# Kernel tuning notes

Measured on AMD Instinct MI355X. Metric: run time of the kernel, lower is better.

Reference implementation:

```python
import jax, jax.numpy as jnp
import numpy as np

N = 32768
F0, F1, F2, F3 = 16, 32, 64, 128
D0, D1, D2, D3 = (128, 128, 128), (64, 64, 64), (32, 32, 32), (16, 16, 16)
DST1, DST2, DTF = (16, 16, 16, 64), (64, 64, 32, 16), (4, 4, 4, 65536)
FST1, FST2, FTF = 64, 8, 8
TOTAL = 7 * (F0 + F1 + F2 + F3) + 9 * FST1 + 9 * FST2 + FTF  # 2336
INNER = 64
FACE3 = np.array([[1,0,0],[-1,0,0],[0,1,0],[0,-1,0],[0,0,1],[0,0,-1]], np.int32)
ST8 = np.concatenate([np.concatenate([FACE3, np.zeros((6,1), np.int32)], 1),
                      np.array([[0,0,0,1],[0,0,0,-1]], np.int32)], 0)

def rmsnorm(x, scale, eps=1e-8):
    rms = jnp.sqrt(jnp.mean(x * x, axis=-1, keepdims=True))
    return scale * x / (rms + eps)

def geglu(x):
    a, g = jnp.split(x, 2, axis=-1)
    return a * jax.nn.gelu(g)

def table_feats(table, p, offsets):
    # p in [0,1)^D -> scaled integer indices; gather base + modulo-wrapped neighbors
    dims = np.array(table.shape[:-1], np.int32)
    idx = (p * (dims - 1)).astype(jnp.int32)  # [N, D]
    base = table[tuple(idx[:, i] for i in range(idx.shape[-1]))]  # [N, F]
    if offsets is None:
        return base
    nbr = (idx[:, None, :] + offsets[None]) % dims  # [N, K, D]
    nf = table[tuple(nbr[..., i] for i in range(nbr.shape[-1]))]  # [N, K, F]
    return jnp.concatenate([base, nf.reshape(nf.shape[0], -1)], axis=-1)

def setup_inputs():
    key = jax.random.key(0)
    ks = jax.random.split(key, 20)
    tbl = lambda k, dims, f: jax.random.normal(k, dims + (f,), jnp.float32) * 0.1
    lin = lambda k, i, o: jax.random.normal(k, (i, o), jnp.float32) / np.sqrt(i).astype(np.float32)
    return dict(
        pos=jax.random.normal(ks[0], (N, 3), jnp.float32),
        dir=jax.random.normal(ks[1], (N, 3), jnp.float32),
        t=jax.random.uniform(ks[2], (N,), jnp.float32),
        table0=tbl(ks[3], D0, F0), table1=tbl(ks[4], D1, F1),
        table2=tbl(ks[5], D2, F2), table3=tbl(ks[6], D3, F3),
        st1=tbl(ks[7], DST1, FST1), st2=tbl(ks[8], DST2, FST2), tf=tbl(ks[9], DTF, FTF),
        sph_proj=lin(ks[10], 3, 8), tb1=jnp.zeros((1,), jnp.float32), tb2=jnp.zeros((1,), jnp.float32),
        gn1=jnp.ones((12,), jnp.float32), gw1=lin(ks[11], 12, 32),
        gn2=jnp.ones((16,), jnp.float32), gw2=lin(ks[12], 16, 32),
        gn3=jnp.ones((16,), jnp.float32), gw3=lin(ks[13], 16, 3),
        vn1=jnp.ones((TOTAL,), jnp.float32), vw1=lin(ks[14], TOTAL, 2 * TOTAL),
        vn2=jnp.ones((TOTAL,), jnp.float32), vw2=lin(ks[15], TOTAL, INNER),
        fw=lin(ks[16], INNER + 4, 4), fb=jnp.zeros((4,), jnp.float32))

def _forward(pos, dir, t, table0, table1, table2, table3, st1, st2, tf,
             sph_proj, tb1, tb2, gn1, gw1, gn2, gw2, gn3, gw3,
             vn1, vw1, vn2, vw2, fw, fb):
    # SphericalEmbedding
    rho = jnp.sqrt(jnp.sum(pos * pos, axis=-1, keepdims=True))
    phi = jnp.arctan2(pos[:, 1], pos[:, 0])
    theta = jnp.arccos(jnp.clip(pos[:, 2] / rho[:, 0], -1.0, 1.0))
    sph = jnp.stack([rho[:, 0], phi, theta], axis=-1) @ sph_proj  # [N, 8]
    # TimeEmbedding
    ct = jnp.cos(t[:, None] + tb1)
    st_ = jnp.sin(t[:, None] + tb2)
    temb = jnp.concatenate([ct, st_, jax.nn.silu(ct), jax.nn.silu(st_)], axis=-1)  # [N, 4]
    # geometric projection MLP -> normalized lookup coords
    h = jnp.concatenate([sph, temb], axis=-1)  # [N, 12]
    h = geglu(rmsnorm(h, gn1) @ gw1)  # [N, 16]
    h = geglu(rmsnorm(h, gn2) @ gw2)  # [N, 16]
    p = jax.nn.sigmoid(rmsnorm(h, gn3) @ gw3)  # [N, 3] in (0,1)
    pt = jnp.concatenate([p, t[:, None]], axis=-1)  # [N, 4]
    # multi-resolution gathers: base + 6 face neighbors per spatial table
    allf = jnp.concatenate([
        table_feats(table0, p, FACE3), table_feats(table1, p, FACE3),
        table_feats(table2, p, FACE3), table_feats(table3, p, FACE3),
        table_feats(st1, pt, ST8), table_feats(st2, pt, ST8),
        table_feats(tf, pt, None)], axis=-1)  # [N, TOTAL]
    # value MLP
    v = geglu(rmsnorm(allf, vn1) @ vw1)  # [N, TOTAL]
    down = rmsnorm(v, vn2) @ vw2  # [N, INNER]
    final_in = jnp.concatenate([down, p, t[:, None]], axis=-1)  # [N, INNER+4]
    return final_in @ fw + fb  # [N, 4]

def reference(pos, dir, t, table0, table1, table2, table3, st1, st2, tf,
              sph_proj, tb1, tb2, gn1, gw1, gn2, gw2, gn3, gw3,
              vn1, vw1, vn2, vw2, fw, fb):
    return _forward(pos, dir, t, table0, table1, table2, table3, st1, st2, tf,
                    sph_proj, tb1, tb2, gn1, gw1, gn2, gw2, gn3, gw3,
                    vn1, vw1, vn2, vw2, fw, fb)
```

## Files before the change

### kernel.cpp

```cpp
#include <hip/hip_runtime.h>
#include <hip/hip_bf16.h>
#include <stdint.h>

typedef __hip_bfloat16 bf16;
typedef __attribute__((ext_vector_type(8))) short v8s;
typedef __attribute__((ext_vector_type(4))) float v4f;

#define NPTS 32768
#define KTOT 2336
#define MPH  2368

#define AS1C(p) ((const __attribute__((address_space(1))) void*)(p))
#define AS3(p)  ((__attribute__((address_space(3))) void*)(p))

__device__ __forceinline__ float sigm(float x){ return 1.0f/(1.0f + expf(-x)); }
__device__ __forceinline__ float gelu_tanh(float x){
  float u = 0.7978845608028654f*(x + 0.044715f*x*x*x);
  return 0.5f*x*(1.0f + tanhf(u));
}
__device__ __forceinline__ float bf2f(uint16_t h){
  union{uint32_t u; float f;} c; c.u = ((uint32_t)h)<<16; return c.f;
}

__global__ __launch_bounds__(256) void k_preamble(
    const float* __restrict__ pos, const float* __restrict__ t,
    const float* __restrict__ sph_proj, const float* __restrict__ tb1,
    const float* __restrict__ tb2,
    const float* __restrict__ gn1, const float* __restrict__ gw1,
    const float* __restrict__ gn2, const float* __restrict__ gw2,
    const float* __restrict__ gn3, const float* __restrict__ gw3,
    float4* __restrict__ Pbuf)
{
  int i = blockIdx.x*256 + threadIdx.x;
  if(i >= NPTS) return;
  float px = pos[3*i], py = pos[3*i+1], pz = pos[3*i+2];
  float rho = sqrtf(px*px + py*py + pz*pz);
  float phi = atan2f(py, px);
  float cz = fminf(1.0f, fmaxf(-1.0f, pz/rho));
  float theta = acosf(cz);
  float tv = t[i];
  float h[12];
  #pragma unroll
  for(int j=0;j<8;j++)
    h[j] = rho*sph_proj[j] + phi*sph_proj[8+j] + theta*sph_proj[16+j];
  float ct = cosf(tv + tb1[0]);
  float st = sinf(tv + tb2[0]);
  h[8]=ct; h[9]=st; h[10]=ct*sigm(ct); h[11]=st*sigm(st);

  float ss = 0.f;
  #pragma unroll
  for(int j=0;j<12;j++) ss += h[j]*h[j];
  float den = sqrtf(ss/12.0f) + 1e-8f;
  float hn[12];
  #pragma unroll
  for(int j=0;j<12;j++) hn[j] = gn1[j]*h[j]/den;

  float h2[16];
  #pragma unroll
  for(int j=0;j<16;j++){
    float a=0.f, g=0.f;
    #pragma unroll
    for(int k=0;k<12;k++){ a += hn[k]*gw1[k*32+j]; g += hn[k]*gw1[k*32+16+j]; }
    h2[j] = a*gelu_tanh(g);
  }
  ss = 0.f;
  #pragma unroll
  for(int j=0;j<16;j++) ss += h2[j]*h2[j];
  den = sqrtf(ss/16.0f) + 1e-8f;
  float hn2[16];
  #pragma unroll
  for(int j=0;j<16;j++) hn2[j] = gn2[j]*h2[j]/den;

  float h3[16];
  #pragma unroll
  for(int j=0;j<16;j++){
    float a=0.f, g=0.f;
    #pragma unroll
    for(int k=0;k<16;k++){ a += hn2[k]*gw2[k*32+j]; g += hn2[k]*gw2[k*32+16+j]; }
    h3[j] = a*gelu_tanh(g);
  }
  ss = 0.f;
  #pragma unroll
  for(int j=0;j<16;j++) ss += h3[j]*h3[j];
  den = sqrtf(ss/16.0f) + 1e-8f;
  float q[3];
  #pragma unroll
  for(int j=0;j<3;j++){
    float a=0.f;
    #pragma unroll
    for(int k=0;k<16;k++) a += (gn3[k]*h3[k]/den)*gw3[k*3+j];
    q[j] = sigm(a);
  }
  Pbuf[i] = make_float4(q[0], q[1], q[2], tv);
}

__device__ __forceinline__ float row_copy(const float* __restrict__ rowp, int F,
                                          bf16* __restrict__ dst, int lane){
  float ss = 0.f;
  for(int f=lane; f<F; f+=64){
    float v = rowp[f];
    dst[f] = __float2bfloat16(v);
    ss += v*v;
  }
  return ss;
}

__device__ __forceinline__ float table3_gather(const float* __restrict__ T, int d, int F,
    float p0, float p1, float p2, bf16* __restrict__ dst, int lane){
  int ix = (int)(p0*(float)(d-1));
  int iy = (int)(p1*(float)(d-1));
  int iz = (int)(p2*(float)(d-1));
  int xp = (ix+1>=d)?0:ix+1, xm = (ix==0)?d-1:ix-1;
  int yp = (iy+1>=d)?0:iy+1, ym = (iy==0)?d-1:iy-1;
  int zp = (iz+1>=d)?0:iz+1, zm = (iz==0)?d-1:iz-1;
  float ss = 0.f;
  ss += row_copy(T + ((size_t)(ix*d+iy)*d+iz)*F, F, dst + 0*F, lane);
  ss += row_copy(T + ((size_t)(xp*d+iy)*d+iz)*F, F, dst + 1*F, lane);
  ss += row_copy(T + ((size_t)(xm*d+iy)*d+iz)*F, F, dst + 2*F, lane);
  ss += row_copy(T + ((size_t)(ix*d+yp)*d+iz)*F, F, dst + 3*F, lane);
  ss += row_copy(T + ((size_t)(ix*d+ym)*d+iz)*F, F, dst + 4*F, lane);
  ss += row_copy(T + ((size_t)(ix*d+iy)*d+zp)*F, F, dst + 5*F, lane);
  ss += row_copy(T + ((size_t)(ix*d+iy)*d+zm)*F, F, dst + 6*F, lane);
  return ss;
}

__device__ __forceinline__ float table4_gather(const float* __restrict__ T,
    int d0,int d1,int d2,int d3,int F,
    float p0,float p1,float p2,float p3, bf16* __restrict__ dst, int lane){
  int ix = (int)(p0*(float)(d0-1));
  int iy = (int)(p1*(float)(d1-1));
  int iz = (int)(p2*(float)(d2-1));
  int iw = (int)(p3*(float)(d3-1));
  int xp=(ix+1>=d0)?0:ix+1, xm=(ix==0)?d0-1:ix-1;
  int yp=(iy+1>=d1)?0:iy+1, ym=(iy==0)?d1-1:iy-1;
  int zp=(iz+1>=d2)?0:iz+1, zm=(iz==0)?d2-1:iz-1;
  int wp=(iw+1>=d3)?0:iw+1, wm=(iw==0)?d3-1:iw-1;
  float ss = 0.f;
  #define RP(x,y,z,w) (T + ((((size_t)(x)*d1 + (y))*d2 + (z))*d3 + (w))*F)
  ss += row_copy(RP(ix,iy,iz,iw), F, dst + 0*F, lane);
  ss += row_copy(RP(xp,iy,iz,iw), F, dst + 1*F, lane);
  ss += row_copy(RP(xm,iy,iz,iw), F, dst + 2*F, lane);
  ss += row_copy(RP(ix,yp,iz,iw), F, dst + 3*F, lane);
  ss += row_copy(RP(ix,ym,iz,iw), F, dst + 4*F, lane);
  ss += row_copy(RP(ix,iy,zp,iw), F, dst + 5*F, lane);
  ss += row_copy(RP(ix,iy,zm,iw), F, dst + 6*F, lane);
  ss += row_copy(RP(ix,iy,iz,wp), F, dst + 7*F, lane);
  ss += row_copy(RP(ix,iy,iz,wm), F, dst + 8*F, lane);
  #undef RP
  return ss;
}

__global__ __launch_bounds__(256) void k_gather(
    const float4* __restrict__ Pbuf,
    const float* __restrict__ T0, const float* __restrict__ T1,
    const float* __restrict__ T2, const float* __restrict__ T3,
    const float* __restrict__ S1, const float* __restrict__ S2,
    const float* __restrict__ TF,
    bf16* __restrict__ X, float* __restrict__ sx)
{
  int wave = threadIdx.x>>6, lane = threadIdx.x&63;
  int ptid = blockIdx.x*4 + wave;
  float4 P = Pbuf[ptid];
  bf16* dst = X + (size_t)ptid*KTOT;
  float ss = 0.f;
  ss += table3_gather(T0, 128, 16, P.x, P.y, P.z, dst + 0,    lane);
  ss += table3_gather(T1,  64, 32, P.x, P.y, P.z, dst + 112,  lane);
  ss += table3_gather(T2,  32, 64, P.x, P.y, P.z, dst + 336,  lane);
  ss += table3_gather(T3,  16,128, P.x, P.y, P.z, dst + 784,  lane);
  ss += table4_gather(S1, 16,16,16,64, 64, P.x,P.y,P.z,P.w, dst + 1680, lane);
  ss += table4_gather(S2, 64,64,32,16,  8, P.x,P.y,P.z,P.w, dst + 2256, lane);
  {
    int ix=(int)(P.x*3.0f), iy=(int)(P.y*3.0f), iz=(int)(P.z*3.0f);
    int iw=(int)(P.w*65535.0f);
    ss += row_copy(TF + (((size_t)((ix*4+iy)*4+iz))*65536 + iw)*8, 8, dst + 2328, lane);
  }
  #pragma unroll
  for(int o=32;o>0;o>>=1) ss += __shfl_xor(ss, o);
  if(lane==0) sx[ptid] = 1.0f/(sqrtf(ss/2336.0f) + 1e-8f);
}

__global__ __launch_bounds__(256) void k_w1prep(const float* __restrict__ vw1,
                                                const float* __restrict__ vn1,
                                                bf16* __restrict__ W1b)
{
  __shared__ float tile[32][33];
  int h  = blockIdx.z;
  int m0 = blockIdx.x*32, k0 = blockIdx.y*32;
  int tx = threadIdx.x & 31, ty = threadIdx.x >> 5;
  #pragma unroll
  for(int dy=0; dy<32; dy+=8){
    int k = k0 + ty + dy;
    tile[ty+dy][tx] = vw1[(size_t)k*4672 + h*2336 + m0 + tx] * vn1[k];
  }
  __syncthreads();
  #pragma unroll
  for(int dy=0; dy<32; dy+=8){
    int m = m0 + ty + dy;
    W1b[(size_t)(h*MPH + m)*KTOT + k0 + tx] = __float2bfloat16(tile[tx][ty+dy]);
  }
}

__global__ __launch_bounds__(256) void k_w1pad(bf16* __restrict__ W1b){
  int idx = blockIdx.x*256 + threadIdx.x;
  const int total = 2*32*KTOT;
  if(idx >= total) return;
  int h = idx / (32*KTOT);
  int r = idx % (32*KTOT);
  int m = 2336 + r / KTOT;
  int k = r % KTOT;
  W1b[(size_t)(h*MPH + m)*KTOT + k] = __float2bfloat16(0.0f);
}

__global__ __launch_bounds__(256) void k_w2prep(const float* __restrict__ vw2,
                                                const float* __restrict__ vn2,
                                                const float* __restrict__ fw,
                                                float4* __restrict__ W2f)
{
  int k = blockIdx.x*256 + threadIdx.x;
  if(k >= KTOT) return;
  float a0=0,a1=0,a2=0,a3=0;
  for(int i=0;i<64;i++){
    float w = vw2[k*64+i];
    a0 += w*fw[i*4+0]; a1 += w*fw[i*4+1]; a2 += w*fw[i*4+2]; a3 += w*fw[i*4+3];
  }
  float s = vn2[k];
  W2f[k] = make_float4(s*a0, s*a1, s*a2, s*a3);
}

__global__ __launch_bounds__(256) void k_gemm1(
    const bf16* __restrict__ X, const bf16* __restrict__ W1b,
    const float* __restrict__ sx, bf16* __restrict__ V)
{
  __shared__ bf16 As[128*32];
  __shared__ bf16 Bs[2*64*32];
  int tid = threadIdx.x;
  int wave = tid>>6, lane = tid&63;
  int bx = blockIdx.x, by = blockIdx.y;
  int row0 = by*128;
  int colh = bx*64;
  int wm = wave>>1, wn = wave&1;
  int lm = lane&15, lq = lane>>4;

  v4f acc[2][4][2];
  #pragma unroll
  for(int h=0;h<2;h++)
    #pragma unroll
    for(int i=0;i<4;i++)
      #pragma unroll
      for(int j=0;j<2;j++)
        acc[h][i][j] = (v4f){0.f,0.f,0.f,0.f};

  const bf16* Xb  = X   + (size_t)row0*KTOT;
  const bf16* Wb0 = W1b + (size_t)colh*KTOT;
  const bf16* Wb1 = W1b + (size_t)(MPH + colh)*KTOT;

  for(int k0=0; k0<KTOT; k0+=32){
    #pragma unroll
    for(int it=0; it<2; it++){
      int c = it*256 + tid;
      const bf16* g = Xb + (size_t)(c>>2)*KTOT + k0 + (c&3)*8;
      __builtin_amdgcn_global_load_lds(AS1C(g), AS3(As + (size_t)(it*256 + wave*64)*8), 16, 0, 0);
    }
    {
      const bf16* g  = Wb0 + (size_t)(tid>>2)*KTOT + k0 + (tid&3)*8;
      __builtin_amdgcn_global_load_lds(AS1C(g),  AS3(Bs + (size_t)(wave*64)*8),       16, 0, 0);
      const bf16* g2 = Wb1 + (size_t)(tid>>2)*KTOT + k0 + (tid&3)*8;
      __builtin_amdgcn_global_load_lds(AS1C(g2), AS3(Bs + (size_t)(256 + wave*64)*8), 16, 0, 0);
    }
    __syncthreads();

    v8s af[4], ba[2], bg[2];
    #pragma unroll
    for(int i=0;i<4;i++){
      int r = wm*64 + i*16 + lm;
      af[i] = *(const v8s*)(As + (size_t)(r*4 + lq)*8);
    }
    #pragma unroll
    for(int j=0;j<2;j++){
      int r = wn*32 + j*16 + lm;
      ba[j] = *(const v8s*)(Bs + (size_t)(r*4 + lq)*8);
      bg[j] = *(const v8s*)(Bs + (size_t)(256*8) + (size_t)(r*4 + lq)*8);
    }
    #pragma unroll
    for(int i=0;i<4;i++)
      #pragma unroll
      for(int j=0;j<2;j++){
        acc[0][i][j] = __builtin_amdgcn_mfma_f32_16x16x32_bf16(af[i], ba[j], acc[0][i][j], 0,0,0);
        acc[1][i][j] = __builtin_amdgcn_mfma_f32_16x16x32_bf16(af[i], bg[j], acc[1][i][j], 0,0,0);
      }
    __syncthreads();
  }

  #pragma unroll
  for(int i=0;i<4;i++){
    #pragma unroll
    for(int r=0;r<4;r++){
      int grow = row0 + wm*64 + i*16 + lq*4 + r;
      float s = sx[grow];
      #pragma unroll
      for(int j=0;j<2;j++){
        int gcol = colh + wn*32 + j*16 + lm;
        float va = s*acc[0][i][j][r];
        float vg = s*acc[1][i][j][r];
        float v = va * gelu_tanh(vg);
        if(gcol < KTOT)
          V[(size_t)grow*KTOT + gcol] = __float2bfloat16(v);
      }
    }
  }
}

__global__ __launch_bounds__(256) void k_rowred(const bf16* __restrict__ V,
                                                float* __restrict__ sv){
  int wave = threadIdx.x>>6, lane = threadIdx.x&63;
  int row = blockIdx.x*4 + wave;
  const uint32_t* Vu = (const uint32_t*)(V + (size_t)row*KTOT);
  float ss = 0.f;
  for(int idx=lane; idx<KTOT/2; idx+=64){
    uint32_t u = Vu[idx];
    float a = bf2f((uint16_t)(u & 0xffffu));
    float b = bf2f((uint16_t)(u >> 16));
    ss += a*a + b*b;
  }
  #pragma unroll
  for(int o=32;o>0;o>>=1) ss += __shfl_xor(ss, o);
  if(lane==0) sv[row] = 1.0f/(sqrtf(ss/2336.0f) + 1e-8f);
}

__global__ __launch_bounds__(256) void k_final(const bf16* __restrict__ V,
    const float* __restrict__ sv, const float4* __restrict__ Pbuf,
    const float4* __restrict__ W2f, const float* __restrict__ fw,
    const float* __restrict__ fb, float4* __restrict__ out)
{
  int wave = threadIdx.x>>6, lane = threadIdx.x&63;
  int p = blockIdx.x*4 + wave;
  const uint32_t* Vu = (const uint32_t*)(V + (size_t)p*KTOT);
  float a0=0,a1=0,a2=0,a3=0;
  for(int idx=lane; idx<KTOT/2; idx+=64){
    uint32_t u = Vu[idx];
    float va = bf2f((uint16_t)(u & 0xffffu));
    float vb = bf2f((uint16_t)(u >> 16));
    float4 w0 = W2f[2*idx], w1 = W2f[2*idx+1];
    a0 += va*w0.x + vb*w1.x;
    a1 += va*w0.y + vb*w1.y;
    a2 += va*w0.z + vb*w1.z;
    a3 += va*w0.w + vb*w1.w;
  }
  #pragma unroll
  for(int o=32;o>0;o>>=1){
    a0 += __shfl_xor(a0,o); a1 += __shfl_xor(a1,o);
    a2 += __shfl_xor(a2,o); a3 += __shfl_xor(a3,o);
  }
  if(lane==0){
    float s = sv[p];
    float4 P = Pbuf[p];
    float o0 = s*a0 + P.x*fw[64*4+0] + P.y*fw[65*4+0] + P.z*fw[66*4+0] + P.w*fw[67*4+0] + fb[0];
    float o1 = s*a1 + P.x*fw[64*4+1] + P.y*fw[65*4+1] + P.z*fw[66*4+1] + P.w*fw[67*4+1] + fb[1];
    float o2 = s*a2 + P.x*fw[64*4+2] + P.y*fw[65*4+2] + P.z*fw[66*4+2] + P.w*fw[67*4+2] + fb[2];
    float o3 = s*a3 + P.x*fw[64*4+3] + P.y*fw[65*4+3] + P.z*fw[66*4+3] + P.w*fw[67*4+3] + fb[3];
    out[p] = make_float4(o0,o1,o2,o3);
  }
}

extern "C" void kernel_launch(void* const* d_in, const int* in_sizes, int n_in,
                              void* d_out, int out_size, void* d_ws, size_t ws_size,
                              hipStream_t stream)
{
  const float* pos = (const float*)d_in[0];
  const float* t   = (const float*)d_in[2];
  const float* T0  = (const float*)d_in[3];
  const float* T1  = (const float*)d_in[4];
  const float* T2  = (const float*)d_in[5];
  const float* T3  = (const float*)d_in[6];
  const float* S1  = (const float*)d_in[7];
  const float* S2  = (const float*)d_in[8];
  const float* TF  = (const float*)d_in[9];
  const float* sph = (const float*)d_in[10];
  const float* tb1 = (const float*)d_in[11];
  const float* tb2 = (const float*)d_in[12];
  const float* gn1 = (const float*)d_in[13];
  const float* gw1 = (const float*)d_in[14];
  const float* gn2 = (const float*)d_in[15];
  const float* gw2 = (const float*)d_in[16];
  const float* gn3 = (const float*)d_in[17];
  const float* gw3 = (const float*)d_in[18];
  const float* vn1 = (const float*)d_in[19];
  const float* vw1 = (const float*)d_in[20];
  const float* vn2 = (const float*)d_in[21];
  const float* vw2 = (const float*)d_in[22];
  const float* fw  = (const float*)d_in[23];
  const float* fb  = (const float*)d_in[24];

  uint8_t* ws = (uint8_t*)d_ws;
  size_t off = 0;
  auto carve = [&](size_t bytes)->void*{
    void* pp = ws + off; off += (bytes + 255) & ~(size_t)255; return pp;
  };
  float4* Pbuf = (float4*)carve((size_t)NPTS*sizeof(float4));
  float*  sx   = (float*) carve((size_t)NPTS*sizeof(float));
  float*  sv   = (float*) carve((size_t)NPTS*sizeof(float));
  float4* W2f  = (float4*)carve((size_t)KTOT*sizeof(float4));
  bf16*   W1b  = (bf16*)  carve((size_t)2*MPH*KTOT*sizeof(bf16));
  bf16*   X    = (bf16*)  carve((size_t)NPTS*KTOT*sizeof(bf16));
  bf16*   V    = (bf16*)  carve((size_t)NPTS*KTOT*sizeof(bf16));

  k_preamble<<<NPTS/256, 256, 0, stream>>>(pos, t, sph, tb1, tb2,
                                           gn1, gw1, gn2, gw2, gn3, gw3, Pbuf);
  k_gather<<<NPTS/4, 256, 0, stream>>>(Pbuf, T0, T1, T2, T3, S1, S2, TF, X, sx);
  k_w1prep<<<dim3(73,73,2), 256, 0, stream>>>(vw1, vn1, W1b);
  k_w1pad<<<(2*32*KTOT + 255)/256, 256, 0, stream>>>(W1b);
  k_w2prep<<<(KTOT + 255)/256, 256, 0, stream>>>(vw2, vn2, fw, W2f);
  k_gemm1<<<dim3(37, 256), 256, 0, stream>>>(X, W1b, sx, V);
  k_rowred<<<NPTS/4, 256, 0, stream>>>(V, sv);
  k_final<<<NPTS/4, 256, 0, stream>>>(V, sv, Pbuf, W2f, fw, fb, (float4*)d_out);
}
```

Measured before the change: 1.816 ms.

## Fuse down-projection and row-norm reduction into GEMM epilogue, drop V buffer

The GEMM epilogue now computes the geglu output and immediately reduces it against the folded second-layer weights and squared norm, writing small per-column-block partials instead of a full bf16 V matrix. A finalize kernel sums the partials and applies the norm and output layer, replacing the rowred and final kernels. This removes a large write and two reads of the intermediate activation. The change also adds an XOR swizzle on LDS tiles, a sigmoid-form gelu approximation, and templated gather copies. The fast gelu and the fp32 partial sums change rounding slightly.

Result: no change. 1.791 ms (-1.4%).

```diff
diff --git a/kernel.cpp b/kernel.cpp
--- a/kernel.cpp
+++ b/kernel.cpp
@@ -9,6 +9,7 @@
 #define NPTS 32768
 #define KTOT 2336
 #define MPH  2368
+#define NBX  37
 
 #define AS1C(p) ((const __attribute__((address_space(1))) void*)(p))
 #define AS3(p)  ((__attribute__((address_space(3))) void*)(p))
@@ -18,8 +19,9 @@
   float u = 0.7978845608028654f*(x + 0.044715f*x*x*x);
   return 0.5f*x*(1.0f + tanhf(u));
 }
-__device__ __forceinline__ float bf2f(uint16_t h){
-  union{uint32_t u; float f;} c; c.u = ((uint32_t)h)<<16; return c.f;
+__device__ __forceinline__ float gelu_fast(float x){
+  float u = 1.5957691216057308f*x*(1.0f + 0.044715f*x*x);
+  return x / (1.0f + __expf(-u));
 }
 
 __global__ __launch_bounds__(256) void k_preamble(
@@ -94,18 +96,39 @@
   Pbuf[i] = make_float4(q[0], q[1], q[2], tv);
 }
 
-__device__ __forceinline__ float row_copy(const float* __restrict__ rowp, int F,
-                                          bf16* __restrict__ dst, int lane){
+template<int F, int R>
+__device__ __forceinline__ float rows_copyT(const float* __restrict__ T,
+    const int (&offs)[R], bf16* __restrict__ dst, int lane){
   float ss = 0.f;
-  for(int f=lane; f<F; f+=64){
-    float v = rowp[f];
-    dst[f] = __float2bfloat16(v);
-    ss += v*v;
+  if constexpr (F >= 64){
+    #pragma unroll
+    for(int r=0;r<R;r++){
+      #pragma unroll
+      for(int f0=0; f0<F; f0+=64){
+        float v = T[(size_t)offs[r] + f0 + lane];
+        dst[r*F + f0 + lane] = __float2bfloat16(v);
+        ss += v*v;
+      }
+    }
+  } else {
+    constexpr int RPP = 64/F;
+    int sub = lane / F;
+    int f   = lane & (F-1);
+    #pragma unroll
+    for(int r0=0;r0<R;r0+=RPP){
+      int r = r0 + sub;
+      if(r < R){
+        float v = T[(size_t)offs[r] + f];
+        dst[r*F + f] = __float2bfloat16(v);
+        ss += v*v;
+      }
+    }
   }
   return ss;
 }
 
-__device__ __forceinline__ float table3_gather(const float* __restrict__ T, int d, int F,
+template<int F>
+__device__ __forceinline__ float table3_gather(const float* __restrict__ T, int d,
     float p0, float p1, float p2, bf16* __restrict__ dst, int lane){
   int ix = (int)(p0*(float)(d-1));
   int iy = (int)(p1*(float)(d-1));
@@ -113,19 +136,16 @@
   int xp = (ix+1>=d)?0:ix+1, xm = (ix==0)?d-1:ix-1;
   int yp = (iy+1>=d)?0:iy+1, ym = (iy==0)?d-1:iy-1;
   int zp = (iz+1>=d)?0:iz+1, zm = (iz==0)?d-1:iz-1;
-  float ss = 0.f;
-  ss += row_copy(T + ((size_t)(ix*d+iy)*d+iz)*F, F, dst + 0*F, lane);
-  ss += row_copy(T + ((size_t)(xp*d+iy)*d+iz)*F, F, dst + 1*F, lane);
-  ss += row_copy(T + ((size_t)(xm*d+iy)*d+iz)*F, F, dst + 2*F, lane);
-  ss += row_copy(T + ((size_t)(ix*d+yp)*d+iz)*F, F, dst + 3*F, lane);
-  ss += row_copy(T + ((size_t)(ix*d+ym)*d+iz)*F, F, dst + 4*F, lane);
-  ss += row_copy(T + ((size_t)(ix*d+iy)*d+zp)*F, F, dst + 5*F, lane);
-  ss += row_copy(T + ((size_t)(ix*d+iy)*d+zm)*F, F, dst + 6*F, lane);
-  return ss;
-}
-
+  int offs[7] = {
+    ((ix*d+iy)*d+iz)*F, ((xp*d+iy)*d+iz)*F, ((xm*d+iy)*d+iz)*F,
+    ((ix*d+yp)*d+iz)*F, ((ix*d+ym)*d+iz)*F,
+    ((ix*d+iy)*d+zp)*F, ((ix*d+iy)*d+zm)*F };
+  return rows_copyT<F,7>(T, offs, dst, lane);
+}
+
+template<int F>
 __device__ __forceinline__ float table4_gather(const float* __restrict__ T,
-    int d0,int d1,int d2,int d3,int F,
+    int d0,int d1,int d2,int d3,
     float p0,float p1,float p2,float p3, bf16* __restrict__ dst, int lane){
   int ix = (int)(p0*(float)(d0-1));
   int iy = (int)(p1*(float)(d1-1));
@@ -135,19 +155,13 @@
   int yp=(iy+1>=d1)?0:iy+1, ym=(iy==0)?d1-1:iy-1;
   int zp=(iz+1>=d2)?0:iz+1, zm=(iz==0)?d2-1:iz-1;
   int wp=(iw+1>=d3)?0:iw+1, wm=(iw==0)?d3-1:iw-1;
-  float ss = 0.f;
-  #define RP(x,y,z,w) (T + ((((size_t)(x)*d1 + (y))*d2 + (z))*d3 + (w))*F)
-  ss += row_copy(RP(ix,iy,iz,iw), F, dst + 0*F, lane);
-  ss += row_copy(RP(xp,iy,iz,iw), F, dst + 1*F, lane);
-  ss += row_copy(RP(xm,iy,iz,iw), F, dst + 2*F, lane);
-  ss += row_copy(RP(ix,yp,iz,iw), F, dst + 3*F, lane);
-  ss += row_copy(RP(ix,ym,iz,iw), F, dst + 4*F, lane);
-  ss += row_copy(RP(ix,iy,zp,iw), F, dst + 5*F, lane);
-  ss += row_copy(RP(ix,iy,zm,iw), F, dst + 6*F, lane);
-  ss += row_copy(RP(ix,iy,iz,wp), F, dst + 7*F, lane);
-  ss += row_copy(RP(ix,iy,iz,wm), F, dst + 8*F, lane);
-  #undef RP
-  return ss;
+  #define RO(x,y,z,w) (((((x)*d1 + (y))*d2 + (z))*d3 + (w))*F)
+  int offs[9] = {
+    RO(ix,iy,iz,iw), RO(xp,iy,iz,iw), RO(xm,iy,iz,iw),
+    RO(ix,yp,iz,iw), RO(ix,ym,iz,iw), RO(ix,iy,zp,iw), RO(ix,iy,zm,iw),
+    RO(ix,iy,iz,wp), RO(ix,iy,iz,wm) };
+  #undef RO
+  return rows_copyT<F,9>(T, offs, dst, lane);
 }
 
 __global__ __launch_bounds__(256) void k_gather(
@@ -163,16 +177,17 @@
   float4 P = Pbuf[ptid];
   bf16* dst = X + (size_t)ptid*KTOT;
   float ss = 0.f;
-  ss += table3_gather(T0, 128, 16, P.x, P.y, P.z, dst + 0,    lane);
-  ss += table3_gather(T1,  64, 32, P.x, P.y, P.z, dst + 112,  lane);
-  ss += table3_gather(T2,  32, 64, P.x, P.y, P.z, dst + 336,  lane);
-  ss += table3_gather(T3,  16,128, P.x, P.y, P.z, dst + 784,  lane);
-  ss += table4_gather(S1, 16,16,16,64, 64, P.x,P.y,P.z,P.w, dst + 1680, lane);
-  ss += table4_gather(S2, 64,64,32,16,  8, P.x,P.y,P.z,P.w, dst + 2256, lane);
+  ss += table3_gather<16 >(T0, 128, P.x, P.y, P.z, dst + 0,    lane);
+  ss += table3_gather<32 >(T1,  64, P.x, P.y, P.z, dst + 112,  lane);
+  ss += table3_gather<64 >(T2,  32, P.x, P.y, P.z, dst + 336,  lane);
+  ss += table3_gather<128>(T3,  16, P.x, P.y, P.z, dst + 784,  lane);
+  ss += table4_gather<64>(S1, 16,16,16,64, P.x,P.y,P.z,P.w, dst + 1680, lane);
+  ss += table4_gather<8 >(S2, 64,64,32,16, P.x,P.y,P.z,P.w, dst + 2256, lane);
   {
     int ix=(int)(P.x*3.0f), iy=(int)(P.y*3.0f), iz=(int)(P.z*3.0f);
     int iw=(int)(P.w*65535.0f);
-    ss += row_copy(TF + (((size_t)((ix*4+iy)*4+iz))*65536 + iw)*8, 8, dst + 2328, lane);
+    int offs[1] = { (int)((((ix*4+iy)*4+iz))*65536 + iw)*8 };
+    ss += rows_copyT<8,1>(TF, offs, dst + 2328, lane);
   }
   #pragma unroll
   for(int o=32;o>0;o>>=1) ss += __shfl_xor(ss, o);
@@ -229,7 +244,8 @@
 
 __global__ __launch_bounds__(256) void k_gemm1(
     const bf16* __restrict__ X, const bf16* __restrict__ W1b,
-    const float* __restrict__ sx, bf16* __restrict__ V)
+    const float* __restrict__ sx, const float4* __restrict__ W2f,
+    float* __restrict__ Part)
 {
   __shared__ bf16 As[128*32];
   __shared__ bf16 Bs[2*64*32];
@@ -254,32 +270,42 @@
   const bf16* Wb0 = W1b + (size_t)colh*KTOT;
   const bf16* Wb1 = W1b + (size_t)(MPH + colh)*KTOT;
 
+  int arow0 = (0*256+tid)>>2, aq0 = ((0*256+tid)&3) ^ (((0*256+tid)>>3)&3);
+  int arow1 = (1*256+tid)>>2, aq1 = ((1*256+tid)&3) ^ (((1*256+tid)>>3)&3);
+  int brow  = tid>>2,         bq  = (tid&3) ^ ((tid>>3)&3);
+
+  int aoff[4], boff[2];
+  #pragma unroll
+  for(int i=0;i<4;i++){
+    int r = wm*64 + i*16 + lm;
+    aoff[i] = (r*4 + (lq ^ ((r>>1)&3)))*8;
+  }
+  #pragma unroll
+  for(int j=0;j<2;j++){
+    int r = wn*32 + j*16 + lm;
+    boff[j] = (r*4 + (lq ^ ((r>>1)&3)))*8;
+  }
+
   for(int k0=0; k0<KTOT; k0+=32){
-    #pragma unroll
-    for(int it=0; it<2; it++){
-      int c = it*256 + tid;
-      const bf16* g = Xb + (size_t)(c>>2)*KTOT + k0 + (c&3)*8;
-      __builtin_amdgcn_global_load_lds(AS1C(g), AS3(As + (size_t)(it*256 + wave*64)*8), 16, 0, 0);
-    }
     {
-      const bf16* g  = Wb0 + (size_t)(tid>>2)*KTOT + k0 + (tid&3)*8;
-      __builtin_amdgcn_global_load_lds(AS1C(g),  AS3(Bs + (size_t)(wave*64)*8),       16, 0, 0);
-      const bf16* g2 = Wb1 + (size_t)(tid>>2)*KTOT + k0 + (tid&3)*8;
-      __builtin_amdgcn_global_load_lds(AS1C(g2), AS3(Bs + (size_t)(256 + wave*64)*8), 16, 0, 0);
+      const bf16* g0 = Xb + (size_t)arow0*KTOT + k0 + aq0*8;
+      __builtin_amdgcn_global_load_lds(AS1C(g0), AS3(As + (size_t)(wave*64)*8), 16, 0, 0);
+      const bf16* g1 = Xb + (size_t)arow1*KTOT + k0 + aq1*8;
+      __builtin_amdgcn_global_load_lds(AS1C(g1), AS3(As + (size_t)(256 + wave*64)*8), 16, 0, 0);
+      const bf16* g2 = Wb0 + (size_t)brow*KTOT + k0 + bq*8;
+      __builtin_amdgcn_global_load_lds(AS1C(g2), AS3(Bs + (size_t)(wave*64)*8), 16, 0, 0);
+      const bf16* g3 = Wb1 + (size_t)brow*KTOT + k0 + bq*8;
+      __builtin_amdgcn_global_load_lds(AS1C(g3), AS3(Bs + (size_t)(256 + wave*64)*8), 16, 0, 0);
     }
     __syncthreads();
 
     v8s af[4], ba[2], bg[2];
     #pragma unroll
-    for(int i=0;i<4;i++){
-      int r = wm*64 + i*16 + lm;
-      af[i] = *(const v8s*)(As + (size_t)(r*4 + lq)*8);
-    }
+    for(int i=0;i<4;i++) af[i] = *(const v8s*)(As + aoff[i]);
     #pragma unroll
     for(int j=0;j<2;j++){
-      int r = wn*32 + j*16 + lm;
-      ba[j] = *(const v8s*)(Bs + (size_t)(r*4 + lq)*8);
-      bg[j] = *(const v8s*)(Bs + (size_t)(256*8) + (size_t)(r*4 + lq)*8);
+      ba[j] = *(const v8s*)(Bs + boff[j]);
+      bg[j] = *(const v8s*)(Bs + 2048 + boff[j]);
     }
     #pragma unroll
     for(int i=0;i<4;i++)
@@ -291,75 +317,76 @@
     __syncthreads();
   }
 
-  #pragma unroll
-  for(int i=0;i<4;i++){
-    #pragma unroll
-    for(int r=0;r<4;r++){
-      int grow = row0 + wm*64 + i*16 + lq*4 + r;
-      float s = sx[grow];
+  float* red = (float*)As;
+  #pragma unroll
+  for(int ph=0; ph<2; ph++){
+    if(wn == ph){
       #pragma unroll
-      for(int j=0;j<2;j++){
-        int gcol = colh + wn*32 + j*16 + lm;
-        float va = s*acc[0][i][j][r];
-        float vg = s*acc[1][i][j][r];
-        float v = va * gelu_tanh(vg);
-        if(gcol < KTOT)
-          V[(size_t)grow*KTOT + gcol] = __float2bfloat16(v);
+      for(int i=0;i<4;i++){
+        #pragma unroll
+        for(int r=0;r<4;r++){
+          int lrow = wm*64 + i*16 + lq*4 + r;
+          float s = sx[row0 + lrow];
+          float d0=0,d1=0,d2=0,d3=0,ssq=0;
+          #pragma unroll
+          for(int j=0;j<2;j++){
+            int gcol = colh + wn*32 + j*16 + lm;
+            float va = s*acc[0][i][j][r];
+            float vg = s*acc[1][i][j][r];
+            float v  = va * gelu_fast(vg);
+            int ci = gcol < KTOT ? gcol : KTOT-1;
+            float4 w = W2f[ci];
+            d0 += v*w.x; d1 += v*w.y; d2 += v*w.z; d3 += v*w.w;
+            ssq += v*v;
+          }
+          #pragma unroll
+          for(int o=1;o<16;o<<=1){
+            d0 += __shfl_xor(d0,o); d1 += __shfl_xor(d1,o);
+            d2 += __shfl_xor(d2,o); d3 += __shfl_xor(d3,o);
+            ssq += __shfl_xor(ssq,o);
+          }
+          if(lm==0){
+            if(ph==0){
+              red[lrow*8+0]=d0; red[lrow*8+1]=d1; red[lrow*8+2]=d2;
+              red[lrow*8+3]=d3; red[lrow*8+4]=ssq;
+              red[lrow*8+5]=0.f; red[lrow*8+6]=0.f; red[lrow*8+7]=0.f;
+            } else {
+              red[lrow*8+0]+=d0; red[lrow*8+1]+=d1; red[lrow*8+2]+=d2;
+              red[lrow*8+3]+=d3; red[lrow*8+4]+=ssq;
+            }
+          }
+        }
       }
     }
-  }
-}
-
-__global__ __launch_bounds__(256) void k_rowred(const bf16* __restrict__ V,
-                                                float* __restrict__ sv){
-  int wave = threadIdx.x>>6, lane = threadIdx.x&63;
-  int row = blockIdx.x*4 + wave;
-  const uint32_t* Vu = (const uint32_t*)(V + (size_t)row*KTOT);
-  float ss = 0.f;
-  for(int idx=lane; idx<KTOT/2; idx+=64){
-    uint32_t u = Vu[idx];
-    float a = bf2f((uint16_t)(u & 0xffffu));
-    float b = bf2f((uint16_t)(u >> 16));
-    ss += a*a + b*b;
-  }
-  #pragma unroll
-  for(int o=32;o>0;o>>=1) ss += __shfl_xor(ss, o);
-  if(lane==0) sv[row] = 1.0f/(sqrtf(ss/2336.0f) + 1e-8f);
-}
-
-__global__ __launch_bounds__(256) void k_final(const bf16* __restrict__ V,
-    const float* __restrict__ sv, const float4* __restrict__ Pbuf,
-    const float4* __restrict__ W2f, const float* __restrict__ fw,
+    __syncthreads();
+  }
+  {
+    int rr = tid >> 1, c4 = (tid & 1)*4;
+    float4 val = *(float4*)&red[rr*8 + c4];
+    *(float4*)&Part[((size_t)bx*NPTS + row0 + rr)*8 + c4] = val;
+  }
+}
+
+__global__ __launch_bounds__(256) void k_finalize(const float* __restrict__ Part,
+    const float4* __restrict__ Pbuf, const float* __restrict__ fw,
     const float* __restrict__ fb, float4* __restrict__ out)
 {
-  int wave = threadIdx.x>>6, lane = threadIdx.x&63;
-  int p = blockIdx.x*4 + wave;
-  const uint32_t* Vu = (const uint32_t*)(V + (size_t)p*KTOT);
-  float a0=0,a1=0,a2=0,a3=0;
-  for(int idx=lane; idx<KTOT/2; idx+=64){
-    uint32_t u = Vu[idx];
-    float va = bf2f((uint16_t)(u & 0xffffu));
-    float vb = bf2f((uint16_t)(u >> 16));
-    float4 w0 = W2f[2*idx], w1 = W2f[2*idx+1];
-    a0 += va*w0.x + vb*w1.x;
-    a1 += va*w0.y + vb*w1.y;
-    a2 += va*w0.z + vb*w1.z;
-    a3 += va*w0.w + vb*w1.w;
-  }
-  #pragma unroll
-  for(int o=32;o>0;o>>=1){
-    a0 += __shfl_xor(a0,o); a1 += __shfl_xor(a1,o);
-    a2 += __shfl_xor(a2,o); a3 += __shfl_xor(a3,o);
-  }
-  if(lane==0){
-    float s = sv[p];
-    float4 P = Pbuf[p];
-    float o0 = s*a0 + P.x*fw[64*4+0] + P.y*fw[65*4+0] + P.z*fw[66*4+0] + P.w*fw[67*4+0] + fb[0];
-    float o1 = s*a1 + P.x*fw[64*4+1] + P.y*fw[65*4+1] + P.z*fw[66*4+1] + P.w*fw[67*4+1] + fb[1];
-    float o2 = s*a2 + P.x*fw[64*4+2] + P.y*fw[65*4+2] + P.z*fw[66*4+2] + P.w*fw[67*4+2] + fb[2];
-    float o3 = s*a3 + P.x*fw[64*4+3] + P.y*fw[65*4+3] + P.z*fw[66*4+3] + P.w*fw[67*4+3] + fb[3];
-    out[p] = make_float4(o0,o1,o2,o3);
-  }
+  int row = blockIdx.x*256 + threadIdx.x;
+  const float4* P4 = (const float4*)Part;
+  float d0=0,d1=0,d2=0,d3=0,ss=0;
+  for(int bx=0; bx<NBX; bx++){
+    size_t base = ((size_t)bx*NPTS + row)*2;
+    float4 a = P4[base];
+    float4 b = P4[base+1];
+    d0+=a.x; d1+=a.y; d2+=a.z; d3+=a.w; ss+=b.x;
+  }
+  float sv = 1.0f/(sqrtf(ss/2336.0f)+1e-8f);
+  float4 P = Pbuf[row];
+  float o0 = sv*d0 + P.x*fw[256+0] + P.y*fw[260+0] + P.z*fw[264+0] + P.w*fw[268+0] + fb[0];
+  float o1 = sv*d1 + P.x*fw[256+1] + P.y*fw[260+1] + P.z*fw[264+1] + P.w*fw[268+1] + fb[1];
+  float o2 = sv*d2 + P.x*fw[256+2] + P.y*fw[260+2] + P.z*fw[264+2] + P.w*fw[268+2] + fb[2];
+  float o3 = sv*d3 + P.x*fw[256+3] + P.y*fw[260+3] + P.z*fw[264+3] + P.w*fw[268+3] + fb[3];
+  out[row] = make_float4(o0,o1,o2,o3);
 }
 
 extern "C" void kernel_launch(void* const* d_in, const int* in_sizes, int n_in,
@@ -398,11 +425,10 @@
   };
   float4* Pbuf = (float4*)carve((size_t)NPTS*sizeof(float4));
   float*  sx   = (float*) carve((size_t)NPTS*sizeof(float));
-  float*  sv   = (float*) carve((size_t)NPTS*sizeof(float));
   float4* W2f  = (float4*)carve((size_t)KTOT*sizeof(float4));
   bf16*   W1b  = (bf16*)  carve((size_t)2*MPH*KTOT*sizeof(bf16));
   bf16*   X    = (bf16*)  carve((size_t)NPTS*KTOT*sizeof(bf16));
-  bf16*   V    = (bf16*)  carve((size_t)NPTS*KTOT*sizeof(bf16));
+  float*  Part = (float*) carve((size_t)NBX*NPTS*8*sizeof(float));
 
   k_preamble<<<NPTS/256, 256, 0, stream>>>(pos, t, sph, tb1, tb2,
                                            gn1, gw1, gn2, gw2, gn3, gw3, Pbuf);
@@ -410,7 +436,6 @@
   k_w1prep<<<dim3(73,73,2), 256, 0, stream>>>(vw1, vn1, W1b);
   k_w1pad<<<(2*32*KTOT + 255)/256, 256, 0, stream>>>(W1b);
   k_w2prep<<<(KTOT + 255)/256, 256, 0, stream>>>(vw2, vn2, fw, W2f);
-  k_gemm1<<<dim3(37, 256), 256, 0, stream>>>(X, W1b, sx, V);
-  k_rowred<<<NPTS/4, 256, 0, stream>>>(V, sv);
-  k_final<<<NPTS/4, 256, 0, stream>>>(V, sv, Pbuf, W2f, fw, fb, (float4*)d_out);
-}
+  k_gemm1<<<dim3(NBX, 256), 256, 0, stream>>>(X, W1b, sx, W2f, Part);
+  k_finalize<<<NPTS/256, 256, 0, stream>>>(Part, Pbuf, fw, fb, (float4*)d_out);
+}
```
